# Performance work log

Hardware: AMD Instinct MI355X
Metric: run time of the kernel (lower is better)

Reference implementation:

```python
import jax, jax.numpy as jnp
import numpy as np

N_EMBD = 1024
N_HEAD = 16
HEAD = N_EMBD // N_HEAD


def setup_inputs() -> dict:
    key = jax.random.key(0)
    ks = jax.random.split(key, 6)
    B, S = 4, 2048
    scale = 1.0 / np.sqrt(N_EMBD)
    return {
        "x": jax.random.normal(ks[0], (B, S, N_EMBD), dtype=jnp.float32),
        "Wq": jax.random.normal(ks[1], (N_EMBD, N_EMBD), dtype=jnp.float32) * scale,
        "Wk": jax.random.normal(ks[2], (N_EMBD, N_EMBD), dtype=jnp.float32) * scale,
        "Wv": jax.random.normal(ks[3], (N_EMBD, N_EMBD), dtype=jnp.float32) * scale,
        "Wo": jax.random.normal(ks[4], (N_EMBD, N_EMBD), dtype=jnp.float32) * scale,
        "bo": jnp.zeros((N_EMBD,), dtype=jnp.float32),
    }


def reference(x, Wq, Wk, Wv, Wo, bo):
    B, S, _ = x.shape
    # projections; nn.Linear applies x @ W.T but W is random here, so x @ W is equivalent math
    def split_heads(t):  # (B,S,E) -> (B,H,S,D)
        return t.reshape(B, S, N_HEAD, HEAD).transpose(0, 2, 1, 3)

    q = split_heads(x @ Wq)
    k = split_heads(x @ Wk)
    v = split_heads(x @ Wv)
    scores = jnp.einsum("bhqd,bhkd->bhqk", q, k) * (HEAD ** -0.5)
    causal = jnp.tril(jnp.ones((S, S), dtype=bool))
    scores = jnp.where(causal, scores, -jnp.inf)
    weights = jax.nn.softmax(scores, axis=-1)  # dropout p=0 (eval)
    out = jnp.einsum("bhqk,bhkd->bhqd", weights, v)
    out = out.transpose(0, 2, 1, 3).reshape(B, S, N_EMBD)
    return out @ Wo + bo
```

## Files before the change

kernel.cpp:

```cpp
#include <hip/hip_runtime.h>
#include <hip/hip_bf16.h>

typedef unsigned short u16;
typedef unsigned int u32;
typedef __bf16 bf16x8 __attribute__((ext_vector_type(8)));
typedef __bf16 bf16x4t __attribute__((ext_vector_type(4)));
typedef float f32x4 __attribute__((ext_vector_type(4)));
typedef u16 u16x8 __attribute__((ext_vector_type(8)));
typedef u16 u16x4 __attribute__((ext_vector_type(4)));

#define NB 4
#define SEQ 2048
#define EMB 1024
#define NHEAD 16
#define DHEAD 64
#define MTOT (NB*SEQ)

static __device__ __forceinline__ u16 f2bf(float f) {
  union { __bf16 h; u16 u; } cv;
  cv.h = (__bf16)f;
  return cv.u;
}

static __device__ __forceinline__ float fexp2(float x) {
  float r;
  asm("v_exp_f32 %0, %1" : "=v"(r) : "v"(x));
  return r;
}

static __device__ __forceinline__ void gload16(const void* g, void* l) {
  __builtin_amdgcn_global_load_lds((const __attribute__((address_space(1))) void*)g,
                                   (__attribute__((address_space(3))) void*)l, 16, 0, 0);
}


__global__ __launch_bounds__(256) void k_cvt_x(const float* __restrict__ in, u16* __restrict__ out) {
  size_t i = (size_t)blockIdx.x * 256 + threadIdx.x;
  const float4* p = (const float4*)in + i * 2;
  float4 a = p[0], b = p[1];
  u16x8 r;
  r[0] = f2bf(a.x); r[1] = f2bf(a.y); r[2] = f2bf(a.z); r[3] = f2bf(a.w);
  r[4] = f2bf(b.x); r[5] = f2bf(b.y); r[6] = f2bf(b.z); r[7] = f2bf(b.w);
  *(u16x8*)(out + i * 8) = r;
}

__global__ __launch_bounds__(256) void k_wtrans(const float* __restrict__ W0, const float* __restrict__ W1,
                                                const float* __restrict__ W2, const float* __restrict__ W3,
                                                u16* __restrict__ O0, u16* __restrict__ O1,
                                                u16* __restrict__ O2, u16* __restrict__ O3) {
  __shared__ float tile[64][65];
  const float* W = blockIdx.z == 0 ? W0 : blockIdx.z == 1 ? W1 : blockIdx.z == 2 ? W2 : W3;
  u16* O       = blockIdx.z == 0 ? O0 : blockIdx.z == 1 ? O1 : blockIdx.z == 2 ? O2 : O3;
  const int c0 = blockIdx.x * 64, r0 = blockIdx.y * 64;
  const int t = threadIdx.x;
  const int tr = t >> 4, tc = (t & 15) * 4;
#pragma unroll
  for (int p = 0; p < 4; p++) {
    int r = tr + p * 16;
    float4 v = *(const float4*)&W[(size_t)(r0 + r) * EMB + c0 + tc];
    tile[r][tc + 0] = v.x; tile[r][tc + 1] = v.y; tile[r][tc + 2] = v.z; tile[r][tc + 3] = v.w;
  }
  __syncthreads();
#pragma unroll
  for (int p = 0; p < 4; p++) {
    int orow = tr + p * 16;
    u16x4 o;
    o[0] = f2bf(tile[tc + 0][orow]); o[1] = f2bf(tile[tc + 1][orow]);
    o[2] = f2bf(tile[tc + 2][orow]); o[3] = f2bf(tile[tc + 3][orow]);
    *(u16x4*)&O[(size_t)(c0 + orow) * EMB + r0 + tc] = o;
  }
}


static __device__ __forceinline__ void gemm_core(const u16* __restrict__ A, const u16* __restrict__ BT,
                                                 int m0, int n0, f32x4 acc[4][4]) {
  __shared__ u16 As[128 * 64];
  __shared__ u16 Bs[128 * 64];
  const int t = threadIdx.x, l = t & 63, w = t >> 6;
  const int g = l >> 4, q = l & 15;
  const int wm = (w >> 1) * 64, wn = (w & 1) * 64;
  char* AsB = (char*)As; char* BsB = (char*)Bs;

  const f32x4 zero4 = {0.f, 0.f, 0.f, 0.f};
#pragma unroll
  for (int mi = 0; mi < 4; mi++)
#pragma unroll
    for (int ni = 0; ni < 4; ni++) acc[mi][ni] = zero4;

  int srow[4], skel[4];
#pragma unroll
  for (int i = 0; i < 4; i++) {
    int row = w * 32 + i * 8 + (l >> 3);
    int c = (l & 7) ^ (row & 7);
    srow[i] = row; skel[i] = c * 8;
  }

  for (int k0 = 0; k0 < EMB; k0 += 64) {
#pragma unroll
    for (int i = 0; i < 4; i++) {
      gload16(A + (size_t)(m0 + srow[i]) * EMB + k0 + skel[i], AsB + w * 4096 + i * 1024);
      gload16(BT + (size_t)(n0 + srow[i]) * EMB + k0 + skel[i], BsB + w * 4096 + i * 1024);
    }
    __syncthreads();
#pragma unroll
    for (int kc = 0; kc < 2; kc++) {
      bf16x8 af[4], bfv[4];
#pragma unroll
      for (int mi = 0; mi < 4; mi++) {
        int row = wm + mi * 16 + q;
        af[mi] = *(const bf16x8*)(AsB + row * 128 + (((kc * 4 + g) ^ (row & 7)) << 4));
      }
#pragma unroll
      for (int ni = 0; ni < 4; ni++) {
        int row = wn + ni * 16 + q;
        bfv[ni] = *(const bf16x8*)(BsB + row * 128 + (((kc * 4 + g) ^ (row & 7)) << 4));
      }
#pragma unroll
      for (int mi = 0; mi < 4; mi++)
#pragma unroll
        for (int ni = 0; ni < 4; ni++)
          acc[mi][ni] = __builtin_amdgcn_mfma_f32_16x16x32_bf16(af[mi], bfv[ni], acc[mi][ni], 0, 0, 0);
    }
    __syncthreads();
  }
}

__global__ __launch_bounds__(256) void k_gemm_qkv(const u16* __restrict__ xb,
                                                  const u16* __restrict__ WqT, const u16* __restrict__ WkT,
                                                  const u16* __restrict__ WvT,
                                                  u16* __restrict__ Qb, u16* __restrict__ Kb, u16* __restrict__ Vb) {
  const int z = blockIdx.z;
  const u16* BT = z == 0 ? WqT : (z == 1 ? WkT : WvT);
  u16* Out = z == 0 ? Qb : (z == 1 ? Kb : Vb);
  const float scale = z == 0 ? 0.125f * 1.4426950408889634f : 1.0f;
  const int m0 = blockIdx.y * 128, n0 = blockIdx.x * 128;
  f32x4 acc[4][4];
  gemm_core(xb, BT, m0, n0, acc);
  const int t = threadIdx.x, l = t & 63, w = t >> 6;
  const int g = l >> 4, q = l & 15;
  const int wm = (w >> 1) * 64, wn = (w & 1) * 64;
#pragma unroll
  for (int mi = 0; mi < 4; mi++)
#pragma unroll
    for (int ni = 0; ni < 4; ni++)
#pragma unroll
      for (int jj = 0; jj < 4; jj++) {
        int m = m0 + wm + mi * 16 + g * 4 + jj;
        int n = n0 + wn + ni * 16 + q;
        int b = m >> 11, s = m & 2047;
        int h = n >> 6, d = n & 63;
        Out[(((size_t)(b * NHEAD + h)) * SEQ + s) * DHEAD + d] = f2bf(acc[mi][ni][jj] * scale);
      }
}

__global__ __launch_bounds__(256) void k_gemm_out(const u16* __restrict__ Ob, const u16* __restrict__ WoT,
                                                  const float* __restrict__ bo, float* __restrict__ out) {
  const int m0 = blockIdx.y * 128, n0 = blockIdx.x * 128;
  f32x4 acc[4][4];
  gemm_core(Ob, WoT, m0, n0, acc);
  const int t = threadIdx.x, l = t & 63, w = t >> 6;
  const int g = l >> 4, q = l & 15;
  const int wm = (w >> 1) * 64, wn = (w & 1) * 64;
#pragma unroll
  for (int ni = 0; ni < 4; ni++) {
    int n = n0 + wn + ni * 16 + q;
    float bv = bo[n];
#pragma unroll
    for (int mi = 0; mi < 4; mi++)
#pragma unroll
      for (int jj = 0; jj < 4; jj++) {
        int m = m0 + wm + mi * 16 + g * 4 + jj;
        out[(size_t)m * EMB + n] = acc[mi][ni][jj] + bv;
      }
  }
}

__global__ __launch_bounds__(256, 4) void k_attn(const u16* __restrict__ Qb, const u16* __restrict__ Kb,
                                                 const u16* __restrict__ Vb, u16* __restrict__ Ob) {
  __shared__ u16 Ks[2][64 * 64];
  __shared__ u16 Vt[2][64 * 64];
  __shared__ u16 Ps[4 * 16 * 64];
  const int t = threadIdx.x, l = t & 63, w = t >> 6;
  const int g = l >> 4, q = l & 15;
  const int bh = blockIdx.x;
  const int b = bh >> 4, h = bh & 15;
  const size_t hb = (size_t)bh * SEQ * DHEAD;
  char* PsB = (char*)Ps;
  const float NEG_INF = -__builtin_inff();

  const int i = blockIdx.y;
  const int qA0 = i * 64, qB0 = (31 - i) * 64;
  const int ntA = i + 1, ntB = 32 - i;

  int krow[2], kel[2];
#pragma unroll
  for (int ii = 0; ii < 2; ii++) {
    int row = w * 16 + ii * 8 + (l >> 3);
    krow[ii] = row; kel[ii] = ((l & 7) ^ (row & 7)) * 8;
  }
  const int kp = t & 31, d0v = (t >> 5) * 8;

  auto stageK = [&](int kbase , int bsel) {
    char* dst = (char*)Ks[bsel] + w * 2048;
#pragma unroll
    for (int ii = 0; ii < 2; ii++)
      gload16(Kb + hb + (size_t)(kbase + krow[ii]) * DHEAD + kel[ii], dst + ii * 1024);
  };
  auto loadV = [&](int kbase, u16x8& v0, u16x8& v1) {
    v0 = *(const u16x8*)(Vb + hb + (size_t)(kbase + 2 * kp) * DHEAD + d0v);
    v1 = *(const u16x8*)(Vb + hb + (size_t)(kbase + 2 * kp + 1) * DHEAD + d0v);
  };
  auto writeV = [&](int bsel, const u16x8& v0, const u16x8& v1) {
    char* VtB = (char*)Vt[bsel];
#pragma unroll
    for (int ii = 0; ii < 8; ii++) {
      int d = d0v + ii;
      u32 val = (u32)v0[ii] | ((u32)v1[ii] << 16);
      *(u32*)(VtB + d * 128 + ((kp * 4) ^ ((d & 7) << 4))) = val;
    }
  };

  bf16x8 qfA[2], qfB[2];
#pragma unroll
  for (int kc = 0; kc < 2; kc++) {
    qfA[kc] = *(const bf16x8*)(Qb + hb + (size_t)(qA0 + w * 16 + q) * DHEAD + kc * 32 + g * 8);
    qfB[kc] = *(const bf16x8*)(Qb + hb + (size_t)(qB0 + w * 16 + q) * DHEAD + kc * 32 + g * 8);
  }
  const int qglobA = qA0 + w * 16 + q, qglobB = qB0 + w * 16 + q;

  f32x4 oA[4], oB[4];
  const f32x4 zero4 = {0.f, 0.f, 0.f, 0.f};
#pragma unroll
  for (int df = 0; df < 4; df++) { oA[df] = zero4; oB[df] = zero4; }
  float mA = NEG_INF, lA = 0.f, mB = NEG_INF, lB = 0.f;

  auto compute = [&](const bf16x8 (&qf)[2], f32x4 (&o)[4], float& m_run, float& l_run,
                     bool diag, int qglob, int k0, char* KsB, char* VtB) {
    f32x4 st[4];
#pragma unroll
    for (int kf = 0; kf < 4; kf++) st[kf] = zero4;
    __builtin_amdgcn_s_setprio(1);
#pragma unroll
    for (int kc = 0; kc < 2; kc++)
#pragma unroll
      for (int kf = 0; kf < 4; kf++) {
        int key = kf * 16 + q;
        bf16x8 a = *(const bf16x8*)(KsB + key * 128 + (((kc * 4 + g) ^ (key & 7)) << 4));
        st[kf] = __builtin_amdgcn_mfma_f32_16x16x32_bf16(a, qf[kc], st[kf], 0, 0, 0);
      }
    __builtin_amdgcn_s_setprio(0);

    if (diag) {
#pragma unroll
      for (int kf = 0; kf < 4; kf++)
#pragma unroll
        for (int jj = 0; jj < 4; jj++)
          if (k0 + kf * 16 + g * 4 + jj > qglob) st[kf][jj] = NEG_INF;
    }

    f32x4 mv;
#pragma unroll
    for (int jj = 0; jj < 4; jj++)
      mv[jj] = fmaxf(fmaxf(st[0][jj], st[1][jj]), fmaxf(st[2][jj], st[3][jj]));
    float smax = fmaxf(fmaxf(mv[0], mv[1]), fmaxf(mv[2], mv[3]));
    smax = fmaxf(smax, __shfl_xor(smax, 16));
    smax = fmaxf(smax, __shfl_xor(smax, 32));

    if (!__all(smax - m_run <= 8.0f)) {
      float mnew = fmaxf(m_run, smax);
      float sc = fexp2(m_run - mnew);
      l_run *= sc;
#pragma unroll
      for (int jj = 0; jj < 4; jj++) {
        float scj = __shfl(sc, g * 4 + jj);
#pragma unroll
        for (int df = 0; df < 4; df++) o[df][jj] *= scj;
      }
      m_run = mnew;
    }

    f32x4 pv[4];
#pragma unroll
    for (int kf = 0; kf < 4; kf++)
#pragma unroll
      for (int jj = 0; jj < 4; jj++)
        pv[kf][jj] = fexp2(st[kf][jj] - m_run);
    f32x4 sv = (pv[0] + pv[1]) + (pv[2] + pv[3]);
    float psum = (sv[0] + sv[1]) + (sv[2] + sv[3]);
    psum += __shfl_xor(psum, 16);
    psum += __shfl_xor(psum, 32);
    l_run += psum;

#pragma unroll
    for (int kf = 0; kf < 4; kf++) {
      bf16x4t pk = { (__bf16)pv[kf][0], (__bf16)pv[kf][1], (__bf16)pv[kf][2], (__bf16)pv[kf][3] };
      *(bf16x4t*)(PsB + w * 2048 + q * 128 + ((kf * 32 + g * 8) ^ ((q & 7) << 4))) = pk;
    }
    asm volatile("" ::: "memory");

    __builtin_amdgcn_s_setprio(1);
#pragma unroll
    for (int kc = 0; kc < 2; kc++) {
      bf16x8 pa = *(const bf16x8*)(PsB + w * 2048 + q * 128 + ((kc * 64 + g * 16) ^ ((q & 7) << 4)));
#pragma unroll
      for (int df = 0; df < 4; df++) {
        int d = df * 16 + q;
        bf16x8 vb = *(const bf16x8*)(VtB + d * 128 + (((kc * 4 + g) ^ (d & 7)) << 4));
        o[df] = __builtin_amdgcn_mfma_f32_16x16x32_bf16(pa, vb, o[df], 0, 0, 0);
      }
    }
    __builtin_amdgcn_s_setprio(0);
    asm volatile("" ::: "memory");
  };

  {
    u16x8 v0, v1;
    stageK(0, 0);
    loadV(0, v0, v1);
    writeV(0, v0, v1);
  }
  __syncthreads();

  int buf = 0;
  for (int kt = 0; kt < ntB; ++kt) {
    const int k0 = kt * 64;
    const bool pf = (kt + 1 < ntB);
    u16x8 nv0, nv1;
    if (pf) {
      stageK((kt + 1) * 64, buf ^ 1);
      loadV((kt + 1) * 64, nv0, nv1);
    }
    char* KsB = (char*)Ks[buf];
    char* VtB = (char*)Vt[buf];

    compute(qfB, oB, mB, lB, kt == ntB - 1, qglobB, k0, KsB, VtB);
    if (kt < ntA)
      compute(qfA, oA, mA, lA, kt == ntA - 1, qglobA, k0, KsB, VtB);

    if (pf) writeV(buf ^ 1, nv0, nv1);
    __syncthreads();
    buf ^= 1;
  }

  auto store = [&](f32x4 (&o)[4], float l_run, int q0) {
    float inv = 1.f / l_run;
#pragma unroll
    for (int jj = 0; jj < 4; jj++) {
      float r = __shfl(inv, g * 4 + jj);
      int s = q0 + w * 16 + g * 4 + jj;
#pragma unroll
      for (int df = 0; df < 4; df++)
        Ob[((size_t)(b * SEQ + s)) * EMB + h * DHEAD + df * 16 + q] = f2bf(o[df][jj] * r);
    }
  };
  store(oA, lA, qA0);
  store(oB, lB, qB0);
}


extern "C" void kernel_launch(void* const* d_in, const int* in_sizes, int n_in,
                              void* d_out, int out_size, void* d_ws, size_t ws_size,
                              hipStream_t stream) {
  const float* x  = (const float*)d_in[0];
  const float* Wq = (const float*)d_in[1];
  const float* Wk = (const float*)d_in[2];
  const float* Wv = (const float*)d_in[3];
  const float* Wo = (const float*)d_in[4];
  const float* bo = (const float*)d_in[5];
  float* out = (float*)d_out;

  char* ws = (char*)d_ws;
  u16* xb  = (u16*)(ws);
  u16* WqT = (u16*)(ws + (16u << 20));
  u16* WkT = WqT + (size_t)EMB * EMB;
  u16* WvT = WkT + (size_t)EMB * EMB;
  u16* WoT = WvT + (size_t)EMB * EMB;
  u16* Qb  = (u16*)(ws + (24u << 20));
  u16* Kb  = Qb + (size_t)MTOT * EMB;
  u16* Vb  = Kb + (size_t)MTOT * EMB;
  u16* Ob  = Vb + (size_t)MTOT * EMB;

  k_cvt_x<<<dim3(4096), 256, 0, stream>>>(x, xb);
  k_wtrans<<<dim3(16, 16, 4), 256, 0, stream>>>(Wq, Wk, Wv, Wo, WqT, WkT, WvT, WoT);
  k_gemm_qkv<<<dim3(8, 64, 3), 256, 0, stream>>>(xb, WqT, WkT, WvT, Qb, Kb, Vb);
  k_attn<<<dim3(64, 16), 256, 0, stream>>>(Qb, Kb, Vb, Ob);
  k_gemm_out<<<dim3(8, 64), 256, 0, stream>>>(Ob, WoT, bo, out);
}
```

Baseline: 181.2 us.

## Double-buffer GEMM LDS tiles and remap GEMM blocks for XCD-aware scheduling

The shared GEMM core now double-buffers the A/B LDS tiles, prefetching the next K-slice with direct-to-LDS loads while MFMAs run on the current one. It uses explicit vmcnt waits, raw barriers and raised wave priority around the MFMA block. The QKV and output GEMMs switch to a 1D grid with a block-index remap that groups tiles by wg&7, presumably so work lands per XCD to improve L2 reuse. QKV treats WqT/WkT/WvT as one contiguous weight matrix, relying on them being adjacent in the workspace. The cost is doubled LDS per block (64KB), which may reduce occupancy.

New measurement: 176.5 us. 1.03x faster.

```diff
diff --git a/kernel.cpp b/kernel.cpp
--- a/kernel.cpp
+++ b/kernel.cpp
@@ -74,12 +74,11 @@
 
 static __device__ __forceinline__ void gemm_core(const u16* __restrict__ A, const u16* __restrict__ BT,
                                                  int m0, int n0, f32x4 acc[4][4]) {
-  __shared__ u16 As[128 * 64];
-  __shared__ u16 Bs[128 * 64];
+  __shared__ u16 As[2][128 * 64];
+  __shared__ u16 Bs[2][128 * 64];
   const int t = threadIdx.x, l = t & 63, w = t >> 6;
   const int g = l >> 4, q = l & 15;
   const int wm = (w >> 1) * 64, wn = (w & 1) * 64;
-  char* AsB = (char*)As; char* BsB = (char*)Bs;
 
   const f32x4 zero4 = {0.f, 0.f, 0.f, 0.f};
 #pragma unroll
@@ -91,17 +90,22 @@
 #pragma unroll
   for (int i = 0; i < 4; i++) {
     int row = w * 32 + i * 8 + (l >> 3);
-    int c = (l & 7) ^ (row & 7);
-    srow[i] = row; skel[i] = c * 8;
-  }
-
-  for (int k0 = 0; k0 < EMB; k0 += 64) {
+    srow[i] = row; skel[i] = ((l & 7) ^ (row & 7)) * 8;
+  }
+
+  auto stage = [&](int k0, int bsel) {
+    char* AsB = (char*)As[bsel] + w * 4096;
+    char* BsB = (char*)Bs[bsel] + w * 4096;
 #pragma unroll
     for (int i = 0; i < 4; i++) {
-      gload16(A + (size_t)(m0 + srow[i]) * EMB + k0 + skel[i], AsB + w * 4096 + i * 1024);
-      gload16(BT + (size_t)(n0 + srow[i]) * EMB + k0 + skel[i], BsB + w * 4096 + i * 1024);
-    }
-    __syncthreads();
+      gload16(A + (size_t)(m0 + srow[i]) * EMB + k0 + skel[i], AsB + i * 1024);
+      gload16(BT + (size_t)(n0 + srow[i]) * EMB + k0 + skel[i], BsB + i * 1024);
+    }
+  };
+
+  auto compute = [&](int bsel) {
+    char* AsB = (char*)As[bsel];
+    char* BsB = (char*)Bs[bsel];
 #pragma unroll
     for (int kc = 0; kc < 2; kc++) {
       bf16x8 af[4], bfv[4];
@@ -115,27 +119,49 @@
         int row = wn + ni * 16 + q;
         bfv[ni] = *(const bf16x8*)(BsB + row * 128 + (((kc * 4 + g) ^ (row & 7)) << 4));
       }
+      __builtin_amdgcn_s_setprio(1);
 #pragma unroll
       for (int mi = 0; mi < 4; mi++)
 #pragma unroll
         for (int ni = 0; ni < 4; ni++)
           acc[mi][ni] = __builtin_amdgcn_mfma_f32_16x16x32_bf16(af[mi], bfv[ni], acc[mi][ni], 0, 0, 0);
-    }
-    __syncthreads();
-  }
-}
-
-__global__ __launch_bounds__(256) void k_gemm_qkv(const u16* __restrict__ xb,
-                                                  const u16* __restrict__ WqT, const u16* __restrict__ WkT,
-                                                  const u16* __restrict__ WvT,
+      __builtin_amdgcn_s_setprio(0);
+    }
+  };
+
+  stage(0, 0);
+  int buf = 0;
+  for (int k0 = 64; k0 <= EMB; k0 += 64) {
+    const bool pf = (k0 < EMB);
+    if (pf) {
+      stage(k0, buf ^ 1);
+      asm volatile("s_waitcnt vmcnt(8)" ::: "memory");
+    } else {
+      asm volatile("s_waitcnt vmcnt(0)" ::: "memory");
+    }
+    __builtin_amdgcn_s_barrier();
+    __builtin_amdgcn_sched_barrier(0);
+    compute(buf);
+    asm volatile("s_waitcnt lgkmcnt(0)" ::: "memory");
+    __builtin_amdgcn_s_barrier();
+    buf ^= 1;
+  }
+}
+
+__global__ __launch_bounds__(256) void k_gemm_qkv(const u16* __restrict__ xb, const u16* __restrict__ Wqkv,
                                                   u16* __restrict__ Qb, u16* __restrict__ Kb, u16* __restrict__ Vb) {
-  const int z = blockIdx.z;
-  const u16* BT = z == 0 ? WqT : (z == 1 ? WkT : WvT);
+  const int wg = blockIdx.x;
+  const int c = wg & 7, local = wg >> 3;
+  const int mi_ = local & 63, ni_ = c * 3 + (local >> 6);
+  const int m0 = mi_ * 128, n0 = ni_ * 128;
+
+  f32x4 acc[4][4];
+  gemm_core(xb, Wqkv, m0, n0, acc);
+
+  const int z = n0 >> 10;
   u16* Out = z == 0 ? Qb : (z == 1 ? Kb : Vb);
   const float scale = z == 0 ? 0.125f * 1.4426950408889634f : 1.0f;
-  const int m0 = blockIdx.y * 128, n0 = blockIdx.x * 128;
-  f32x4 acc[4][4];
-  gemm_core(xb, BT, m0, n0, acc);
+
   const int t = threadIdx.x, l = t & 63, w = t >> 6;
   const int g = l >> 4, q = l & 15;
   const int wm = (w >> 1) * 64, wn = (w & 1) * 64;
@@ -148,16 +174,21 @@
         int m = m0 + wm + mi * 16 + g * 4 + jj;
         int n = n0 + wn + ni * 16 + q;
         int b = m >> 11, s = m & 2047;
-        int h = n >> 6, d = n & 63;
+        int col = n & 1023;
+        int h = col >> 6, d = col & 63;
         Out[(((size_t)(b * NHEAD + h)) * SEQ + s) * DHEAD + d] = f2bf(acc[mi][ni][jj] * scale);
       }
 }
 
 __global__ __launch_bounds__(256) void k_gemm_out(const u16* __restrict__ Ob, const u16* __restrict__ WoT,
                                                   const float* __restrict__ bo, float* __restrict__ out) {
-  const int m0 = blockIdx.y * 128, n0 = blockIdx.x * 128;
+  const int wg = blockIdx.x;
+  const int c = wg & 7, local = wg >> 3;
+  const int m0 = (local & 63) * 128, n0 = c * 128;
+
   f32x4 acc[4][4];
   gemm_core(Ob, WoT, m0, n0, acc);
+
   const int t = threadIdx.x, l = t & 63, w = t >> 6;
   const int g = l >> 4, q = l & 15;
   const int wm = (w >> 1) * 64, wn = (w & 1) * 64;
@@ -200,7 +231,7 @@
   }
   const int kp = t & 31, d0v = (t >> 5) * 8;
 
-  auto stageK = [&](int kbase , int bsel) {
+  auto stageK = [&](int kbase, int bsel) {
     char* dst = (char*)Ks[bsel] + w * 2048;
 #pragma unroll
     for (int ii = 0; ii < 2; ii++)
@@ -382,7 +413,7 @@
 
   k_cvt_x<<<dim3(4096), 256, 0, stream>>>(x, xb);
   k_wtrans<<<dim3(16, 16, 4), 256, 0, stream>>>(Wq, Wk, Wv, Wo, WqT, WkT, WvT, WoT);
-  k_gemm_qkv<<<dim3(8, 64, 3), 256, 0, stream>>>(xb, WqT, WkT, WvT, Qb, Kb, Vb);
+  k_gemm_qkv<<<dim3(1536), 256, 0, stream>>>(xb, WqT, Qb, Kb, Vb);
   k_attn<<<dim3(64, 16), 256, 0, stream>>>(Qb, Kb, Vb, Ob);
-  k_gemm_out<<<dim3(8, 64), 256, 0, stream>>>(Ob, WoT, bo, out);
-}
+  k_gemm_out<<<dim3(512), 256, 0, stream>>>(Ob, WoT, bo, out);
+}
```
